# Kernel optimization log

Hardware: AMD Instinct MI355X
Metric: run time of the kernel (lower is better)

Reference implementation:

```python
import jax, jax.numpy as jnp
import numpy as np

E, TWO_I, H = 8, 3072, 2048
I = TWO_I // 2
T = 16384

def setup_inputs() -> dict:
    key = jax.random.key(0)
    k1, k2, k3 = jax.random.split(key, 3)
    scale_gu = 1.0 / np.sqrt(H)
    scale_dn = 1.0 / np.sqrt(I)
    return {
        "current_state": jax.random.normal(k1, (T, H), dtype=jnp.float32),
        "gate_up_proj": jax.random.normal(k2, (E, TWO_I, H), dtype=jnp.float32) * scale_gu,
        "down_proj": jax.random.normal(k3, (E, H, I), dtype=jnp.float32) * scale_dn,
        "expert_idx": 3,
    }

def reference(current_state, gate_up_proj, down_proj, expert_idx):
    # F.linear(x, W) == x @ W.T
    w_gu = gate_up_proj[expert_idx]            # [2I, H]
    w_dn = down_proj[expert_idx]               # [H, I]
    gu = jnp.einsum("th,ih->ti", current_state, w_gu)  # [T, 2I]
    gate, up = jnp.split(gu, 2, axis=-1)       # each [T, I]
    hidden = jax.nn.silu(gate) * up            # SwiGLU gating
    return jnp.einsum("ti,hi->th", hidden, w_dn)  # [T, H]
```

## Files before the change

### kernel.cpp

```cpp
#include <hip/hip_runtime.h>
#include <hip/hip_bf16.h>


namespace {

constexpr int T_ = 16384;
constexpr int H_ = 2048;
constexpr int I_ = 1536;

typedef short short8 __attribute__((ext_vector_type(8)));
typedef float f32x4 __attribute__((ext_vector_type(4)));
typedef unsigned short ushort4v __attribute__((ext_vector_type(4)));

__device__ __forceinline__ unsigned short f2bf(float f) {
    union { float f; unsigned u; } v; v.f = f;
    return (unsigned short)((v.u + 0x7FFFu + ((v.u >> 16) & 1u)) >> 16);
}

typedef __attribute__((address_space(1))) const void gvoid;
typedef __attribute__((address_space(3))) void lvoid;
__device__ __forceinline__ void gload16(const void* g, void* l) {
    __builtin_amdgcn_global_load_lds((gvoid*)g, (lvoid*)l, 16, 0, 0);
}

#define SBAR() do { __builtin_amdgcn_s_barrier(); __builtin_amdgcn_sched_barrier(0); } while (0)
#define VMCNT4() do { asm volatile("s_waitcnt vmcnt(4)" ::: "memory"); __builtin_amdgcn_sched_barrier(0); } while (0)
#define VMCNT0() do { asm volatile("s_waitcnt vmcnt(0)" ::: "memory"); __builtin_amdgcn_sched_barrier(0); } while (0)

__global__ void k_cvt(const float* __restrict__ base, const int* __restrict__ eidx,
                      long sliceElems, unsigned short* __restrict__ dst, int n4) {
    const float* src = base + (size_t)(*eidx) * (size_t)sliceElems;
    int i = blockIdx.x * blockDim.x + threadIdx.x;
    const int stride = gridDim.x * blockDim.x;
    for (; i < n4; i += stride) {
        f32x4 v = ((const f32x4*)src)[i];
        ushort4v h = { f2bf(v[0]), f2bf(v[1]), f2bf(v[2]), f2bf(v[3]) };
        ((ushort4v*)dst)[i] = h;
    }
}

__global__ __launch_bounds__(512, 2) void k_gemm1_swiglu(
    const unsigned short* __restrict__ xb, const unsigned short* __restrict__ wgub,
    unsigned short* __restrict__ hidden)
{
    __shared__ unsigned short lds[4 * 16384];

    const int tid  = threadIdx.x;
    const int lane = tid & 63;
    const int wid  = tid >> 6;
    const int wr   = wid >> 2;
    const int wc   = wid & 3;
    const int l15  = lane & 15;
    const int l4   = lane >> 4;

    const int nb = (blockIdx.x & 7) * 96 + (blockIdx.x >> 3);
    const int bx = nb % 12, by = nb / 12;
    const int m0 = by * 256;
    const int n0 = bx * 128;

    const int srow = lane >> 2;
    const int scol = (lane & 3) * 8;

    f32x4 acc[8][4];
    #pragma unroll
    for (int m = 0; m < 8; ++m)
        #pragma unroll
        for (int n = 0; n < 4; ++n) acc[m][n] = (f32x4)0.0f;

    constexpr int NT = H_ / 32;

    #pragma unroll
    for (int tt = 0; tt < 2; ++tt) {
        unsigned short* stA = lds + tt * 16384;
        unsigned short* stB = stA + 8192;
        const int kS = tt * 32;
        #pragma unroll
        for (int j = 0; j < 2; ++j) {
            const int rb = (wid * 2 + j) * 16;
            gload16(xb + (size_t)(m0 + rb + srow) * H_ + kS + scol, stA + rb * 32);
        }
        #pragma unroll
        for (int j = 0; j < 2; ++j) {
            const int rb = (wid * 2 + j) * 16;
            const int growb = (rb < 128) ? (n0 + rb) : (I_ + n0 + rb - 128);
            gload16(wgub + (size_t)(growb + srow) * H_ + kS + scol, stB + rb * 32);
        }
    }
    VMCNT4();
    SBAR();

    const int aoff = wr * 4096 + l15 * 32 + l4 * 8;
    const int boff = wc * 2048 + l15 * 32 + l4 * 8;

    for (int t = 0; t < NT; ++t) {
        const unsigned short* bA = lds + (t & 3) * 16384;
        const unsigned short* bB = bA + 8192;
        unsigned short* stA = lds + ((t + 2) & 3) * 16384;
        unsigned short* stB = stA + 8192;
        const int kS = (t + 2) * 32;
        const bool st = (t + 2 < NT);

        short8 bf[4], af[4];
        #pragma unroll
        for (int n = 0; n < 4; ++n) bf[n] = *(const short8*)(bB + boff + n * 512);
        #pragma unroll
        for (int a = 0; a < 4; ++a) af[a] = *(const short8*)(bA + aoff + a * 512);
        if (st) {
            #pragma unroll
            for (int j = 0; j < 2; ++j) {
                const int rb = (wid * 2 + j) * 16;
                gload16(xb + (size_t)(m0 + rb + srow) * H_ + kS + scol, stA + rb * 32);
            }
        }
        SBAR();
        __builtin_amdgcn_s_setprio(1);
        #pragma unroll
        for (int a = 0; a < 4; ++a)
            #pragma unroll
            for (int n = 0; n < 4; ++n)
                acc[a][n] = __builtin_amdgcn_mfma_f32_16x16x32_bf16(af[a], bf[n], acc[a][n], 0, 0, 0);
        __builtin_amdgcn_s_setprio(0);
        SBAR();

        #pragma unroll
        for (int a = 0; a < 4; ++a) af[a] = *(const short8*)(bA + aoff + 2048 + a * 512);
        if (st) {
            #pragma unroll
            for (int j = 0; j < 2; ++j) {
                const int rb = (wid * 2 + j) * 16;
                const int growb = (rb < 128) ? (n0 + rb) : (I_ + n0 + rb - 128);
                gload16(wgub + (size_t)(growb + srow) * H_ + kS + scol, stB + rb * 32);
            }
        }
        SBAR();
        __builtin_amdgcn_s_setprio(1);
        #pragma unroll
        for (int a = 0; a < 4; ++a)
            #pragma unroll
            for (int n = 0; n < 4; ++n)
                acc[4 + a][n] = __builtin_amdgcn_mfma_f32_16x16x32_bf16(af[a], bf[n], acc[4 + a][n], 0, 0, 0);
        __builtin_amdgcn_s_setprio(0);
        if (t < NT - 2)       { VMCNT4(); }
        else if (t == NT - 2) { VMCNT0(); }
        SBAR();
    }

    float* exch = (float*)lds;
    if (wc >= 2) {
        #pragma unroll
        for (int m = 0; m < 8; ++m)
            #pragma unroll
            for (int n = 0; n < 4; ++n)
                #pragma unroll
                for (int j = 0; j < 4; ++j) {
                    const int row = wr * 128 + m * 16 + l4 * 4 + j;
                    const int col = (wc - 2) * 64 + n * 16 + l15;
                    exch[row * 128 + col] = acc[m][n][j];
                }
    }
    __syncthreads();
    if (wc < 2) {
        #pragma unroll
        for (int m = 0; m < 8; ++m)
            #pragma unroll
            for (int n = 0; n < 4; ++n)
                #pragma unroll
                for (int j = 0; j < 4; ++j) {
                    const int row = wr * 128 + m * 16 + l4 * 4 + j;
                    const int col = wc * 64 + n * 16 + l15;
                    const float g = acc[m][n][j];
                    const float u = exch[row * 128 + col];
                    const float s = g / (1.0f + __expf(-g));
                    hidden[(size_t)(m0 + row) * I_ + n0 + col] = f2bf(s * u);
                }
    }
}

__global__ __launch_bounds__(512, 2) void k_gemm2(
    const unsigned short* __restrict__ hidden, const unsigned short* __restrict__ wdnb,
    float* __restrict__ out)
{
    __shared__ unsigned short lds[4 * 16384];

    const int tid  = threadIdx.x;
    const int lane = tid & 63;
    const int wid  = tid >> 6;
    const int wr   = wid >> 2;
    const int wc   = wid & 3;
    const int l15  = lane & 15;
    const int l4   = lane >> 4;

    const int nb = (blockIdx.x & 7) * 64 + (blockIdx.x >> 3);
    const int bx = nb & 7, by = nb >> 3;
    const int m0 = by * 256;
    const int n0 = bx * 256;

    const int srow = lane >> 2;
    const int scol = (lane & 3) * 8;

    f32x4 acc[8][4];
    #pragma unroll
    for (int m = 0; m < 8; ++m)
        #pragma unroll
        for (int n = 0; n < 4; ++n) acc[m][n] = (f32x4)0.0f;

    constexpr int NT = I_ / 32;

    #pragma unroll
    for (int tt = 0; tt < 2; ++tt) {
        unsigned short* stA = lds + tt * 16384;
        unsigned short* stB = stA + 8192;
        const int kS = tt * 32;
        #pragma unroll
        for (int j = 0; j < 2; ++j) {
            const int rb = (wid * 2 + j) * 16;
            gload16(hidden + (size_t)(m0 + rb + srow) * I_ + kS + scol, stA + rb * 32);
        }
        #pragma unroll
        for (int j = 0; j < 2; ++j) {
            const int rb = (wid * 2 + j) * 16;
            gload16(wdnb + (size_t)(n0 + rb + srow) * I_ + kS + scol, stB + rb * 32);
        }
    }
    VMCNT4();
    SBAR();

    const int aoff = wr * 4096 + l15 * 32 + l4 * 8;
    const int boff = wc * 2048 + l15 * 32 + l4 * 8;

    for (int t = 0; t < NT; ++t) {
        const unsigned short* bA = lds + (t & 3) * 16384;
        const unsigned short* bB = bA + 8192;
        unsigned short* stA = lds + ((t + 2) & 3) * 16384;
        unsigned short* stB = stA + 8192;
        const int kS = (t + 2) * 32;
        const bool st = (t + 2 < NT);

        short8 bf[4], af[4];
        #pragma unroll
        for (int n = 0; n < 4; ++n) bf[n] = *(const short8*)(bB + boff + n * 512);
        #pragma unroll
        for (int a = 0; a < 4; ++a) af[a] = *(const short8*)(bA + aoff + a * 512);
        if (st) {
            #pragma unroll
            for (int j = 0; j < 2; ++j) {
                const int rb = (wid * 2 + j) * 16;
                gload16(hidden + (size_t)(m0 + rb + srow) * I_ + kS + scol, stA + rb * 32);
            }
        }
        SBAR();
        __builtin_amdgcn_s_setprio(1);
        #pragma unroll
        for (int a = 0; a < 4; ++a)
            #pragma unroll
            for (int n = 0; n < 4; ++n)
                acc[a][n] = __builtin_amdgcn_mfma_f32_16x16x32_bf16(af[a], bf[n], acc[a][n], 0, 0, 0);
        __builtin_amdgcn_s_setprio(0);
        SBAR();

        #pragma unroll
        for (int a = 0; a < 4; ++a) af[a] = *(const short8*)(bA + aoff + 2048 + a * 512);
        if (st) {
            #pragma unroll
            for (int j = 0; j < 2; ++j) {
                const int rb = (wid * 2 + j) * 16;
                gload16(wdnb + (size_t)(n0 + rb + srow) * I_ + kS + scol, stB + rb * 32);
            }
        }
        SBAR();
        __builtin_amdgcn_s_setprio(1);
        #pragma unroll
        for (int a = 0; a < 4; ++a)
            #pragma unroll
            for (int n = 0; n < 4; ++n)
                acc[4 + a][n] = __builtin_amdgcn_mfma_f32_16x16x32_bf16(af[a], bf[n], acc[4 + a][n], 0, 0, 0);
        __builtin_amdgcn_s_setprio(0);
        if (t < NT - 2)       { VMCNT4(); }
        else if (t == NT - 2) { VMCNT0(); }
        SBAR();
    }

    #pragma unroll
    for (int m = 0; m < 8; ++m)
        #pragma unroll
        for (int n = 0; n < 4; ++n)
            #pragma unroll
            for (int j = 0; j < 4; ++j) {
                const int row = m0 + wr * 128 + m * 16 + l4 * 4 + j;
                const int col = n0 + wc * 64 + n * 16 + l15;
                out[(size_t)row * H_ + col] = acc[m][n][j];
            }
}

}

extern "C" void kernel_launch(void* const* d_in, const int* in_sizes, int n_in,
                              void* d_out, int out_size, void* d_ws, size_t ws_size,
                              hipStream_t stream) {
    const float* x   = (const float*)d_in[0];
    const float* wgu = (const float*)d_in[1];
    const float* wdn = (const float*)d_in[2];
    const int* eidx  = (const int*)d_in[3];
    float* out = (float*)d_out;

    unsigned short* xb     = (unsigned short*)d_out;
    unsigned short* hidden = (unsigned short*)d_ws;
    unsigned short* wgub   = (unsigned short*)((char*)d_ws + 50331648);
    unsigned short* wdnb   = (unsigned short*)((char*)d_ws + 62914560);

    k_cvt<<<2048, 256, 0, stream>>>(x, eidx, 0L, xb, (T_ * H_) / 4);
    k_cvt<<<2048, 256, 0, stream>>>(wgu, eidx, (long)(2 * I_) * H_, wgub, (2 * I_ * H_) / 4);
    k_cvt<<<2048, 256, 0, stream>>>(wdn, eidx, (long)H_ * I_, wdnb, (H_ * I_) / 4);
    k_gemm1_swiglu<<<dim3((T_ / 256) * (I_ / 128)), 512, 0, stream>>>(xb, wgub, hidden);
    k_gemm2<<<dim3((T_ / 256) * (H_ / 256)), 512, 0, stream>>>(hidden, wdnb, out);
}
```

Baseline: 382.4 us.

## Restructure GEMM main loops with register double-buffered fragments and deeper prefetch

Both GEMM kernels replace the two-half-phase loop (four barriers per K-tile) with a single barrier per tile. The loop now prefetches three tiles ahead into a four-slot LDS ring and double-buffers the A/B fragments in registers, so the next tile's LDS reads overlap the current tile's MFMAs. The sched_barrier after the waitcnt macros and the setprio hints are dropped. The SwiGLU up-half exchange through LDS now stores bf16 instead of fp32, which adds rounding of the up value and a risk of higher register pressure at two blocks per CU. There is also a possible race: stage(t+3) writes slot (t+3)&3 == (t-1)&3 while slower waves may still be reading slot t-1 before the barrier.

```diff
diff --git a/kernel.cpp b/kernel.cpp
--- a/kernel.cpp
+++ b/kernel.cpp
@@ -15,6 +15,10 @@
 __device__ __forceinline__ unsigned short f2bf(float f) {
     union { float f; unsigned u; } v; v.f = f;
     return (unsigned short)((v.u + 0x7FFFu + ((v.u >> 16) & 1u)) >> 16);
+}
+__device__ __forceinline__ float bf2f(unsigned short u) {
+    union { unsigned u; float f; } v; v.u = (unsigned)u << 16;
+    return v.f;
 }
 
 typedef __attribute__((address_space(1))) const void gvoid;
@@ -24,8 +28,8 @@
 }
 
 #define SBAR() do { __builtin_amdgcn_s_barrier(); __builtin_amdgcn_sched_barrier(0); } while (0)
-#define VMCNT4() do { asm volatile("s_waitcnt vmcnt(4)" ::: "memory"); __builtin_amdgcn_sched_barrier(0); } while (0)
-#define VMCNT0() do { asm volatile("s_waitcnt vmcnt(0)" ::: "memory"); __builtin_amdgcn_sched_barrier(0); } while (0)
+#define VMCNT4() do { asm volatile("s_waitcnt vmcnt(4)" ::: "memory"); } while (0)
+#define VMCNT0() do { asm volatile("s_waitcnt vmcnt(0)" ::: "memory"); } while (0)
 
 __global__ void k_cvt(const float* __restrict__ base, const int* __restrict__ eidx,
                       long sliceElems, unsigned short* __restrict__ dst, int n4) {
@@ -69,11 +73,13 @@
 
     constexpr int NT = H_ / 32;
 
-    #pragma unroll
-    for (int tt = 0; tt < 2; ++tt) {
-        unsigned short* stA = lds + tt * 16384;
+    const int aoff = wr * 4096 + l15 * 32 + l4 * 8;
+    const int boff = wc * 2048 + l15 * 32 + l4 * 8;
+
+    auto stage = [&](int s) {
+        unsigned short* stA = lds + (s & 3) * 16384;
         unsigned short* stB = stA + 8192;
-        const int kS = tt * 32;
+        const int kS = s * 32;
         #pragma unroll
         for (int j = 0; j < 2; ++j) {
             const int rb = (wid * 2 + j) * 16;
@@ -85,67 +91,42 @@
             const int growb = (rb < 128) ? (n0 + rb) : (I_ + n0 + rb - 128);
             gload16(wgub + (size_t)(growb + srow) * H_ + kS + scol, stB + rb * 32);
         }
-    }
+    };
+    auto readfrags = [&](int s, short8 (&AF)[8], short8 (&BF)[4]) {
+        const unsigned short* bA = lds + (s & 3) * 16384;
+        const unsigned short* bB = bA + 8192;
+        #pragma unroll
+        for (int a = 0; a < 8; ++a) AF[a] = *(const short8*)(bA + aoff + a * 512);
+        #pragma unroll
+        for (int n = 0; n < 4; ++n) BF[n] = *(const short8*)(bB + boff + n * 512);
+    };
+    auto body = [&](int t, short8 (&AF)[8], short8 (&BF)[4],
+                    short8 (&NAF)[8], short8 (&NBF)[4]) {
+        if (t + 3 < NT) stage(t + 3);
+        if (t + 1 < NT) readfrags(t + 1, NAF, NBF);
+        #pragma unroll
+        for (int a = 0; a < 8; ++a)
+            #pragma unroll
+            for (int n = 0; n < 4; ++n)
+                acc[a][n] = __builtin_amdgcn_mfma_f32_16x16x32_bf16(AF[a], BF[n], acc[a][n], 0, 0, 0);
+        if (t + 3 < NT) { VMCNT4(); } else { VMCNT0(); }
+        SBAR();
+    };
+
+    stage(0); stage(1); stage(2);
     VMCNT4();
     SBAR();
 
-    const int aoff = wr * 4096 + l15 * 32 + l4 * 8;
-    const int boff = wc * 2048 + l15 * 32 + l4 * 8;
-
-    for (int t = 0; t < NT; ++t) {
-        const unsigned short* bA = lds + (t & 3) * 16384;
-        const unsigned short* bB = bA + 8192;
-        unsigned short* stA = lds + ((t + 2) & 3) * 16384;
-        unsigned short* stB = stA + 8192;
-        const int kS = (t + 2) * 32;
-        const bool st = (t + 2 < NT);
-
-        short8 bf[4], af[4];
-        #pragma unroll
-        for (int n = 0; n < 4; ++n) bf[n] = *(const short8*)(bB + boff + n * 512);
-        #pragma unroll
-        for (int a = 0; a < 4; ++a) af[a] = *(const short8*)(bA + aoff + a * 512);
-        if (st) {
-            #pragma unroll
-            for (int j = 0; j < 2; ++j) {
-                const int rb = (wid * 2 + j) * 16;
-                gload16(xb + (size_t)(m0 + rb + srow) * H_ + kS + scol, stA + rb * 32);
-            }
-        }
-        SBAR();
-        __builtin_amdgcn_s_setprio(1);
-        #pragma unroll
-        for (int a = 0; a < 4; ++a)
-            #pragma unroll
-            for (int n = 0; n < 4; ++n)
-                acc[a][n] = __builtin_amdgcn_mfma_f32_16x16x32_bf16(af[a], bf[n], acc[a][n], 0, 0, 0);
-        __builtin_amdgcn_s_setprio(0);
-        SBAR();
-
-        #pragma unroll
-        for (int a = 0; a < 4; ++a) af[a] = *(const short8*)(bA + aoff + 2048 + a * 512);
-        if (st) {
-            #pragma unroll
-            for (int j = 0; j < 2; ++j) {
-                const int rb = (wid * 2 + j) * 16;
-                const int growb = (rb < 128) ? (n0 + rb) : (I_ + n0 + rb - 128);
-                gload16(wgub + (size_t)(growb + srow) * H_ + kS + scol, stB + rb * 32);
-            }
-        }
-        SBAR();
-        __builtin_amdgcn_s_setprio(1);
-        #pragma unroll
-        for (int a = 0; a < 4; ++a)
-            #pragma unroll
-            for (int n = 0; n < 4; ++n)
-                acc[4 + a][n] = __builtin_amdgcn_mfma_f32_16x16x32_bf16(af[a], bf[n], acc[4 + a][n], 0, 0, 0);
-        __builtin_amdgcn_s_setprio(0);
-        if (t < NT - 2)       { VMCNT4(); }
-        else if (t == NT - 2) { VMCNT0(); }
-        SBAR();
-    }
-
-    float* exch = (float*)lds;
+    short8 afA[8], bfA[4], afB[8], bfB[4];
+    readfrags(0, afA, bfA);
+
+    for (int t = 0; t < NT; t += 2) {
+        body(t,     afA, bfA, afB, bfB);
+        body(t + 1, afB, bfB, afA, bfA);
+    }
+
+    __syncthreads();
+    unsigned short* exch = lds;
     if (wc >= 2) {
         #pragma unroll
         for (int m = 0; m < 8; ++m)
@@ -155,7 +136,7 @@
                 for (int j = 0; j < 4; ++j) {
                     const int row = wr * 128 + m * 16 + l4 * 4 + j;
                     const int col = (wc - 2) * 64 + n * 16 + l15;
-                    exch[row * 128 + col] = acc[m][n][j];
+                    exch[row * 128 + col] = f2bf(acc[m][n][j]);
                 }
     }
     __syncthreads();
@@ -169,7 +150,7 @@
                     const int row = wr * 128 + m * 16 + l4 * 4 + j;
                     const int col = wc * 64 + n * 16 + l15;
                     const float g = acc[m][n][j];
-                    const float u = exch[row * 128 + col];
+                    const float u = bf2f(exch[row * 128 + col]);
                     const float s = g / (1.0f + __expf(-g));
                     hidden[(size_t)(m0 + row) * I_ + n0 + col] = f2bf(s * u);
                 }
@@ -206,11 +187,13 @@
 
     constexpr int NT = I_ / 32;
 
-    #pragma unroll
-    for (int tt = 0; tt < 2; ++tt) {
-        unsigned short* stA = lds + tt * 16384;
+    const int aoff = wr * 4096 + l15 * 32 + l4 * 8;
+    const int boff = wc * 2048 + l15 * 32 + l4 * 8;
+
+    auto stage = [&](int s) {
+        unsigned short* stA = lds + (s & 3) * 16384;
         unsigned short* stB = stA + 8192;
-        const int kS = tt * 32;
+        const int kS = s * 32;
         #pragma unroll
         for (int j = 0; j < 2; ++j) {
             const int rb = (wid * 2 + j) * 16;
@@ -221,63 +204,38 @@
             const int rb = (wid * 2 + j) * 16;
             gload16(wdnb + (size_t)(n0 + rb + srow) * I_ + kS + scol, stB + rb * 32);
         }
-    }
+    };
+    auto readfrags = [&](int s, short8 (&AF)[8], short8 (&BF)[4]) {
+        const unsigned short* bA = lds + (s & 3) * 16384;
+        const unsigned short* bB = bA + 8192;
+        #pragma unroll
+        for (int a = 0; a < 8; ++a) AF[a] = *(const short8*)(bA + aoff + a * 512);
+        #pragma unroll
+        for (int n = 0; n < 4; ++n) BF[n] = *(const short8*)(bB + boff + n * 512);
+    };
+    auto body = [&](int t, short8 (&AF)[8], short8 (&BF)[4],
+                    short8 (&NAF)[8], short8 (&NBF)[4]) {
+        if (t + 3 < NT) stage(t + 3);
+        if (t + 1 < NT) readfrags(t + 1, NAF, NBF);
+        #pragma unroll
+        for (int a = 0; a < 8; ++a)
+            #pragma unroll
+            for (int n = 0; n < 4; ++n)
+                acc[a][n] = __builtin_amdgcn_mfma_f32_16x16x32_bf16(AF[a], BF[n], acc[a][n], 0, 0, 0);
+        if (t + 3 < NT) { VMCNT4(); } else { VMCNT0(); }
+        SBAR();
+    };
+
+    stage(0); stage(1); stage(2);
     VMCNT4();
     SBAR();
 
-    const int aoff = wr * 4096 + l15 * 32 + l4 * 8;
-    const int boff = wc * 2048 + l15 * 32 + l4 * 8;
-
-    for (int t = 0; t < NT; ++t) {
-        const unsigned short* bA = lds + (t & 3) * 16384;
-        const unsigned short* bB = bA + 8192;
-        unsigned short* stA = lds + ((t + 2) & 3) * 16384;
-        unsigned short* stB = stA + 8192;
-        const int kS = (t + 2) * 32;
-        const bool st = (t + 2 < NT);
-
-        short8 bf[4], af[4];
-        #pragma unroll
-        for (int n = 0; n < 4; ++n) bf[n] = *(const short8*)(bB + boff + n * 512);
-        #pragma unroll
-        for (int a = 0; a < 4; ++a) af[a] = *(const short8*)(bA + aoff + a * 512);
-        if (st) {
-            #pragma unroll
-            for (int j = 0; j < 2; ++j) {
-                const int rb = (wid * 2 + j) * 16;
-                gload16(hidden + (size_t)(m0 + rb + srow) * I_ + kS + scol, stA + rb * 32);
-            }
-        }
-        SBAR();
-        __builtin_amdgcn_s_setprio(1);
-        #pragma unroll
-        for (int a = 0; a < 4; ++a)
-            #pragma unroll
-            for (int n = 0; n < 4; ++n)
-                acc[a][n] = __builtin_amdgcn_mfma_f32_16x16x32_bf16(af[a], bf[n], acc[a][n], 0, 0, 0);
-        __builtin_amdgcn_s_setprio(0);
-        SBAR();
-
-        #pragma unroll
-        for (int a = 0; a < 4; ++a) af[a] = *(const short8*)(bA + aoff + 2048 + a * 512);
-        if (st) {
-            #pragma unroll
-            for (int j = 0; j < 2; ++j) {
-                const int rb = (wid * 2 + j) * 16;
-                gload16(wdnb + (size_t)(n0 + rb + srow) * I_ + kS + scol, stB + rb * 32);
-            }
-        }
-        SBAR();
-        __builtin_amdgcn_s_setprio(1);
-        #pragma unroll
-        for (int a = 0; a < 4; ++a)
-            #pragma unroll
-            for (int n = 0; n < 4; ++n)
-                acc[4 + a][n] = __builtin_amdgcn_mfma_f32_16x16x32_bf16(af[a], bf[n], acc[4 + a][n], 0, 0, 0);
-        __builtin_amdgcn_s_setprio(0);
-        if (t < NT - 2)       { VMCNT4(); }
-        else if (t == NT - 2) { VMCNT0(); }
-        SBAR();
+    short8 afA[8], bfA[4], afB[8], bfB[4];
+    readfrags(0, afA, bfA);
+
+    for (int t = 0; t < NT; t += 2) {
+        body(t,     afA, bfA, afB, bfB);
+        body(t + 1, afB, bfB, afA, bfA);
     }
 
     #pragma unroll
```

New measurement: 370.9 us. 1.03x faster.
